# Performance work log

Hardware: AMD Instinct MI355X
Metric: run time of the kernel (lower is better)

The kernel has to match this reference:

```python
import jax, jax.numpy as jnp
import numpy as np

N_IMG = 1024
N_VIEWS = 90


def _bilinear(img, yi, xi):
    """Bilinear sample img at float coords (yi=row, xi=col); 0 outside (skimage warp cval=0)."""
    n = img.shape[0]
    y0 = jnp.floor(yi)
    x0 = jnp.floor(xi)
    wy = yi - y0
    wx = xi - x0
    y0i = y0.astype(jnp.int32)
    x0i = x0.astype(jnp.int32)

    def get(yy, xx):
        valid = (yy >= 0) & (yy < n) & (xx >= 0) & (xx < n)
        v = img[jnp.clip(yy, 0, n - 1), jnp.clip(xx, 0, n - 1)]
        return jnp.where(valid, v, jnp.zeros((), img.dtype))

    v00 = get(y0i, x0i)
    v01 = get(y0i, x0i + 1)
    v10 = get(y0i + 1, x0i)
    v11 = get(y0i + 1, x0i + 1)
    return (v00 * (1 - wy) * (1 - wx) + v01 * (1 - wy) * wx
            + v10 * wy * (1 - wx) + v11 * wy * wx)


def radon_jax(image, theta_deg):
    """skimage.transform.radon(image, theta, circle=True) equivalent.
    Rotate image by each angle (bilinear, about center = N//2, inverse map as in
    skimage warp) and sum over rows. Returns sinogram [N, n_angles]."""
    n = image.shape[0]
    center = n // 2
    ang = jnp.deg2rad(theta_deg.astype(image.dtype))
    cos_a = jnp.cos(ang)  # [A]
    sin_a = jnp.sin(ang)
    coords = jnp.arange(n, dtype=image.dtype)
    X, Y = jnp.meshgrid(coords, coords)  # X = col (x), Y = row (y), [N, N]

    def rotate_and_sum(ca, sa):
        # inverse map: src = R @ dst (homogeneous, (x, y) order) as in skimage radon
        x_in = ca * X + sa * Y - center * (ca + sa - 1)
        y_in = -sa * X + ca * Y - center * (ca - sa - 1)
        rotated = _bilinear(image, y_in, x_in)  # [N, N]
        return rotated.sum(axis=0)  # sum over rows -> projection [N]

    sino = jax.vmap(rotate_and_sum)(cos_a, sin_a)  # [A, N]
    return sino.T  # [N, A] to match skimage radon layout


def setup_inputs() -> dict:
    key = jax.random.key(0)
    k1, _ = jax.random.split(key)
    x = jax.random.normal(k1, (N_IMG, N_IMG), dtype=jnp.float32)
    theta = jnp.arange(N_VIEWS, dtype=jnp.float32) * 2.0  # 0..178 deg, 2-deg spacing
    return {"x": x, "theta": theta}


def reference(x, theta):
    return radon_jax(x, theta)
```

## Files before the change

### kernel.cpp

```cpp
#include <hip/hip_runtime.h>

#define N_IMG   1024
#define N_VIEWS 90
#define CENTER  512
#define TILE    64
#define NYB     (N_IMG / TILE)
#define NTHREADS 512
#define NWAVES   8
#define YPT      (TILE / NWAVES)
#define TILE_WORDS 9216

typedef float v2f __attribute__((ext_vector_type(2)));

__device__ __forceinline__ void map_coords(float ca, float sa, float cx, float cy,
                                           float Xf, float Yf,
                                           float& x_in, float& y_in) {
    const float fx0 = fmaf(ca, Xf, cx);
    const float fy0 = fmaf(-sa, Xf, cy);
    x_in = fmaf(sa, Yf, fx0);
    y_in = fmaf(ca, Yf, fy0);
}

__device__ __forceinline__ void gload_lds4(const float* g, float* l) {
    __builtin_amdgcn_global_load_lds((const __attribute__((address_space(1))) void*)g,
                                     (__attribute__((address_space(3))) void*)l, 4, 0, 0);
}
__device__ __forceinline__ void gload_lds16(const float* g, float* l) {
    __builtin_amdgcn_global_load_lds((const __attribute__((address_space(1))) void*)g,
                                     (__attribute__((address_space(3))) void*)l, 16, 0, 0);
}

template<int STRIDE>
__device__ __forceinline__ float sample_tile(const float* __restrict__ tile,
                                             float sa, float ca,
                                             float x_in, float y_in, float basef) {
    const float Sf = (float)STRIDE;
    v2f x2 = {x_in, x_in + sa};
    v2f y2 = {y_in, y_in + ca};
    const v2f dx2 = {2.0f * sa, 2.0f * sa};
    const v2f dy2 = {2.0f * ca, 2.0f * ca};
    const v2f S2  = {Sf, Sf};
    const v2f b2  = {basef, basef};
    v2f acc2 = {0.0f, 0.0f};
    #pragma unroll
    for (int p = 0; p < YPT / 2; ++p) {
        v2f x0f = {floorf(x2.x), floorf(x2.y)};
        v2f y0f = {floorf(y2.x), floorf(y2.y)};
        const v2f wx = x2 - x0f;
        const v2f wy = y2 - y0f;
        const v2f lif = y0f * S2 + x0f + b2;
        const int li0 = (int)lif.x;
        const int li1 = (int)lif.y;
        const v2f t00 = {tile[li0],              tile[li1]};
        const v2f t01 = {tile[li0 + 1],          tile[li1 + 1]};
        const v2f t10 = {tile[li0 + STRIDE],     tile[li1 + STRIDE]};
        const v2f t11 = {tile[li0 + STRIDE + 1], tile[li1 + STRIDE + 1]};
        const v2f top = (t01 - t00) * wx + t00;
        const v2f bot = (t11 - t10) * wx + t10;
        acc2 += (bot - top) * wy + top;
        x2 += dx2; y2 += dy2;
    }
    return acc2.x + acc2.y;
}

__global__ __launch_bounds__(NTHREADS) void radon_tile(const float* __restrict__ img,
                                                       const float* __restrict__ theta,
                                                       float* __restrict__ partial,
                                                       float* __restrict__ out,
                                                       int mode) {
    __shared__ float tile[TILE_WORDS];
    __shared__ float fpar[4];
    __shared__ int   ipar[8];

    const int a  = blockIdx.z;
    const int X0 = blockIdx.x * TILE;
    const int Y0 = blockIdx.y * TILE;
    const int tid  = threadIdx.x;
    const int lane = tid & 63;
    const int wv   = tid >> 6;

    if (wv == 0) {
        const float ang = theta[a] * 0.017453292519943295f;
        float sa, ca;
        __sincosf(ang, &sa, &ca);
        const float cx = (float)CENTER * (1.0f - ca - sa);
        const float cy = (float)CENTER * (1.0f - ca + sa);

        float x00, y00, x01, y01, x10, y10, x11, y11;
        map_coords(ca, sa, cx, cy, (float)X0,        (float)Y0,        x00, y00);
        map_coords(ca, sa, cx, cy, (float)(X0 + 63), (float)Y0,        x01, y01);
        map_coords(ca, sa, cx, cy, (float)X0,        (float)(Y0 + 63), x10, y10);
        map_coords(ca, sa, cx, cy, (float)(X0 + 63), (float)(Y0 + 63), x11, y11);
        const float xmin = fminf(fminf(x00, x01), fminf(x10, x11));
        const float xmax = fmaxf(fmaxf(x00, x01), fmaxf(x10, x11));
        const float ymin = fminf(fminf(y00, y01), fminf(y10, y11));
        const float ymax = fmaxf(fmaxf(y00, y01), fmaxf(y10, y11));

        const int ix0_raw = (int)floorf(xmin);
        const int ix1_raw = (int)floorf(xmax) + 1;
        const int iy0_raw = (int)floorf(ymin);
        const int iy1_raw = (int)floorf(ymax) + 1;

        const bool empty = (ix1_raw < 0) || (ix0_raw > N_IMG - 1) ||
                           (iy1_raw < 0) || (iy0_raw > N_IMG - 1);
        const bool interior = (ix0_raw >= 0) && (ix1_raw <= N_IMG - 1) &&
                              (iy0_raw >= 0) && (iy1_raw <= N_IMG - 1);

        int path = (fabsf(ca) > 0.7072f) ? 0 : ((ca > 0.0f) ? 1 : 2);
        int iy0w, win, dB = 0, ry0 = 0, nrows = 0;
        if (interior) {
            iy0w = iy0_raw;
            if (path == 0) {
                win = min(ix0_raw & ~3, N_IMG - 96);
            } else {
                win = min(ix0_raw, N_IMG - 64);
                dB  = max(win, ix1_raw - 63) - win;
            }
            nrows = iy1_raw - iy0_raw + 1;
        } else {
            iy0w = iy0_raw;
            win  = ix0_raw & ~3;
            ry0  = max(0, iy0_raw);
            nrows = min(N_IMG - 1, iy1_raw) - ry0 + 1;
        }
        if (tid == 0) {
            fpar[0] = sa; fpar[1] = ca; fpar[2] = cx; fpar[3] = cy;
            ipar[0] = iy0w; ipar[1] = nrows; ipar[2] = win; ipar[3] = dB;
            ipar[4] = path;
            ipar[5] = empty ? 1 : (interior ? 2 : 0);
            ipar[6] = ry0;
        }
    }
    __syncthreads();

    float* __restrict__ pslot = partial + ((size_t)(a * NYB + blockIdx.y) << 10) + X0;
    const int flags = ipar[5];

    if (flags & 1) {
        if (mode == 0 && tid < 64) pslot[tid] = 0.0f;
        return;
    }

    const float sa = fpar[0], ca = fpar[1], cx = fpar[2], cy = fpar[3];
    const int iy0 = ipar[0], nrows = ipar[1], win = ipar[2], dB = ipar[3];
    const int path = ipar[4];
    const int S = (path == 0) ? 96 : ((path == 1) ? 95 : 97);

    if (flags & 2) {
        if (path == 0) {
            const int D = nrows * 96;
            for (int o = wv * 256; o < D; o += NWAVES * 256) {
                const int d = o + 4 * lane;
                const int r = (unsigned)d / 96u;
                const int c = d - r * 96;
                const int gr = min(iy0 + r, N_IMG - 1);
                gload_lds16(img + (size_t)gr * N_IMG + win + c, tile + o);
            }
        } else {
            const float* g = img + (size_t)(iy0 + wv) * N_IMG + win + lane;
            float* l = tile + wv * S;
            for (int r = wv; r < nrows; r += NWAVES) {
                gload_lds4(g, l);
                if (dB > 0) gload_lds4(g + dB, l + dB);
                g += NWAVES * N_IMG;
                l += NWAVES * S;
            }
        }
    } else {
        for (int o4 = tid; o4 < TILE_WORDS / 4; o4 += NTHREADS)
            *(float4*)(tile + 4 * o4) = make_float4(0.f, 0.f, 0.f, 0.f);
        __syncthreads();
        const int ry0 = ipar[6];
        const int cx0 = max(0, win);
        const int cxe = min(N_IMG - 1, win + 94);
        const int wIn = cxe - cx0 + 1;
        const int n4  = wIn >> 2;
        const int items = nrows * 24;
        for (int idx = tid; idx < items; idx += NTHREADS) {
            const int r  = (unsigned)idx / 24u;
            const int c4 = idx - r * 24;
            const int gy = ry0 + r;
            float* dst = tile + (gy - iy0) * S + (cx0 - win) + 4 * c4;
            const float* src = img + (size_t)gy * N_IMG + cx0 + 4 * c4;
            if (c4 < n4) {
                *(float4*)dst = *(const float4*)src;
            } else if (c4 == n4) {
                for (int j = 0; j < (wIn & 3); ++j) dst[j] = src[j];
            }
        }
    }
    __syncthreads();

    const float Xf  = (float)(X0 + lane);
    const float fx0 = fmaf(ca, Xf, cx);
    const float fy0 = fmaf(-sa, Xf, cy);
    const float Ybf = (float)(Y0 + wv * YPT);
    const float x_in = fmaf(sa, Ybf, fx0);
    const float y_in = fmaf(ca, Ybf, fy0);
    const float basef = -(float)(iy0 * S + win);

    float acc;
    if (path == 0)      acc = sample_tile<96>(tile, sa, ca, x_in, y_in, basef);
    else if (path == 1) acc = sample_tile<95>(tile, sa, ca, x_in, y_in, basef);
    else                acc = sample_tile<97>(tile, sa, ca, x_in, y_in, basef);

    __syncthreads();
    tile[wv * 64 + lane] = acc;
    __syncthreads();
    if (wv == 0) {
        float s = 0.0f;
        #pragma unroll
        for (int w = 0; w < NWAVES; ++w) s += tile[w * 64 + lane];
        if (mode == 0) pslot[lane] = s;
        else           atomicAdd(&out[(X0 + lane) * N_VIEWS + a], s);
    }
}

__global__ __launch_bounds__(256) void reduce_partials(const float* __restrict__ partial,
                                                       float* __restrict__ out) {
    const int g = blockIdx.x * 256 + threadIdx.x;
    const int a = g >> 10;
    const int X = g & 1023;
    float s = 0.0f;
    #pragma unroll
    for (int yb = 0; yb < NYB; ++yb)
        s += partial[((size_t)(a * NYB + yb) << 10) + X];
    out[X * N_VIEWS + a] = s;
}

extern "C" void kernel_launch(void* const* d_in, const int* in_sizes, int n_in,
                              void* d_out, int out_size, void* d_ws, size_t ws_size,
                              hipStream_t stream) {
    const float* img   = (const float*)d_in[0];
    const float* theta = (const float*)d_in[1];
    float* out     = (float*)d_out;
    float* partial = (float*)d_ws;

    const size_t needed = (size_t)N_VIEWS * NYB * N_IMG * sizeof(float);
    const int mode = (ws_size >= needed) ? 0 : 1;
    if (mode == 1)
        (void)hipMemsetAsync(d_out, 0, (size_t)out_size * sizeof(float), stream);

    dim3 grid(N_IMG / TILE, N_IMG / TILE, N_VIEWS);
    radon_tile<<<grid, NTHREADS, 0, stream>>>(img, theta, partial, out, mode);

    if (mode == 0)
        reduce_partials<<<(N_VIEWS * N_IMG) / 256, 256, 0, stream>>>(partial, out);
}
```

Measured before the change: 140.0 us.

## Use transposed image copy for steep-angle tiles to avoid LDS bank conflicts

Adds a transpose kernel that writes a transposed copy of the image into workspace. For interior tiles whose angle would use the odd-stride paths and whose per-lane offsets would cause bank conflicts, the tile is now loaded from the transposed image with 16-byte global-to-LDS loads and a stride-96 layout. A transposed sampler swaps the x/y roles. This targets LDS bank conflicts and narrow 4-byte loads on near-vertical angles, at the cost of an extra transpose launch and more workspace.

```diff
diff --git a/kernel.cpp b/kernel.cpp
--- a/kernel.cpp
+++ b/kernel.cpp
@@ -28,6 +28,22 @@
 __device__ __forceinline__ void gload_lds16(const float* g, float* l) {
     __builtin_amdgcn_global_load_lds((const __attribute__((address_space(1))) void*)g,
                                      (__attribute__((address_space(3))) void*)l, 16, 0, 0);
+}
+
+__global__ __launch_bounds__(256) void transpose_img(const float* __restrict__ in,
+                                                     float* __restrict__ outT) {
+    __shared__ float t[32][33];
+    const int bx = blockIdx.x * 32;
+    const int by = blockIdx.y * 32;
+    const int lx = threadIdx.x & 31;
+    const int ly = threadIdx.x >> 5;
+    #pragma unroll
+    for (int i = 0; i < 32; i += 8)
+        t[ly + i][lx] = in[(size_t)(by + ly + i) * N_IMG + bx + lx];
+    __syncthreads();
+    #pragma unroll
+    for (int i = 0; i < 32; i += 8)
+        outT[(size_t)(bx + ly + i) * N_IMG + by + lx] = t[lx][ly + i];
 }
 
 template<int STRIDE>
@@ -63,11 +79,45 @@
     return acc2.x + acc2.y;
 }
 
+template<int STRIDE>
+__device__ __forceinline__ float sample_tileT(const float* __restrict__ tile,
+                                              float sa, float ca,
+                                              float x_in, float y_in, float basef) {
+    const float Sf = (float)STRIDE;
+    v2f x2 = {x_in, x_in + sa};
+    v2f y2 = {y_in, y_in + ca};
+    const v2f dx2 = {2.0f * sa, 2.0f * sa};
+    const v2f dy2 = {2.0f * ca, 2.0f * ca};
+    const v2f S2  = {Sf, Sf};
+    const v2f b2  = {basef, basef};
+    v2f acc2 = {0.0f, 0.0f};
+    #pragma unroll
+    for (int p = 0; p < YPT / 2; ++p) {
+        v2f x0f = {floorf(x2.x), floorf(x2.y)};
+        v2f y0f = {floorf(y2.x), floorf(y2.y)};
+        const v2f wx = x2 - x0f;
+        const v2f wy = y2 - y0f;
+        const v2f lif = x0f * S2 + y0f + b2;
+        const int li0 = (int)lif.x;
+        const int li1 = (int)lif.y;
+        const v2f t00 = {tile[li0],              tile[li1]};
+        const v2f t10 = {tile[li0 + 1],          tile[li1 + 1]};
+        const v2f t01 = {tile[li0 + STRIDE],     tile[li1 + STRIDE]};
+        const v2f t11 = {tile[li0 + STRIDE + 1], tile[li1 + STRIDE + 1]};
+        const v2f lft = (t10 - t00) * wy + t00;
+        const v2f rgt = (t11 - t01) * wy + t01;
+        acc2 += (rgt - lft) * wx + lft;
+        x2 += dx2; y2 += dy2;
+    }
+    return acc2.x + acc2.y;
+}
+
 __global__ __launch_bounds__(NTHREADS) void radon_tile(const float* __restrict__ img,
+                                                       const float* __restrict__ imgT,
                                                        const float* __restrict__ theta,
                                                        float* __restrict__ partial,
                                                        float* __restrict__ out,
-                                                       int mode) {
+                                                       int mode, int useT) {
     __shared__ float tile[TILE_WORDS];
     __shared__ float fpar[4];
     __shared__ int   ipar[8];
@@ -107,9 +157,9 @@
                               (iy0_raw >= 0) && (iy1_raw <= N_IMG - 1);
 
         int path = (fabsf(ca) > 0.7072f) ? 0 : ((ca > 0.0f) ? 1 : 2);
-        int iy0w, win, dB = 0, ry0 = 0, nrows = 0;
+        int row0, win, dB = 0, ry0 = 0, nrows = 0;
         if (interior) {
-            iy0w = iy0_raw;
+            row0 = iy0_raw;
             if (path == 0) {
                 win = min(ix0_raw & ~3, N_IMG - 96);
             } else {
@@ -117,15 +167,26 @@
                 dB  = max(win, ix1_raw - 63) - win;
             }
             nrows = iy1_raw - iy0_raw + 1;
+            if (useT && path != 0) {
+                const float tt = (96.0f * ca - sa) * 0.03125f;
+                const float fr = fabsf(tt - rintf(tt)) * 32.0f;
+                if (fr >= 1.0f) {
+                    path  = 3;
+                    row0  = ix0_raw;
+                    nrows = ix1_raw - ix0_raw + 1;
+                    win   = min(iy0_raw & ~3, N_IMG - 96);
+                    dB    = 0;
+                }
+            }
         } else {
-            iy0w = iy0_raw;
+            row0 = iy0_raw;
             win  = ix0_raw & ~3;
             ry0  = max(0, iy0_raw);
             nrows = min(N_IMG - 1, iy1_raw) - ry0 + 1;
         }
         if (tid == 0) {
             fpar[0] = sa; fpar[1] = ca; fpar[2] = cx; fpar[3] = cy;
-            ipar[0] = iy0w; ipar[1] = nrows; ipar[2] = win; ipar[3] = dB;
+            ipar[0] = row0; ipar[1] = nrows; ipar[2] = win; ipar[3] = dB;
             ipar[4] = path;
             ipar[5] = empty ? 1 : (interior ? 2 : 0);
             ipar[6] = ry0;
@@ -142,22 +203,23 @@
     }
 
     const float sa = fpar[0], ca = fpar[1], cx = fpar[2], cy = fpar[3];
-    const int iy0 = ipar[0], nrows = ipar[1], win = ipar[2], dB = ipar[3];
+    const int row0 = ipar[0], nrows = ipar[1], win = ipar[2], dB = ipar[3];
     const int path = ipar[4];
-    const int S = (path == 0) ? 96 : ((path == 1) ? 95 : 97);
+    const int S = (path == 1) ? 95 : ((path == 2) ? 97 : 96);
 
     if (flags & 2) {
-        if (path == 0) {
+        if (path == 0 || path == 3) {
+            const float* src = (path == 0) ? img : imgT;
             const int D = nrows * 96;
             for (int o = wv * 256; o < D; o += NWAVES * 256) {
                 const int d = o + 4 * lane;
                 const int r = (unsigned)d / 96u;
                 const int c = d - r * 96;
-                const int gr = min(iy0 + r, N_IMG - 1);
-                gload_lds16(img + (size_t)gr * N_IMG + win + c, tile + o);
+                const int gr = min(row0 + r, N_IMG - 1);
+                gload_lds16(src + (size_t)gr * N_IMG + win + c, tile + o);
             }
         } else {
-            const float* g = img + (size_t)(iy0 + wv) * N_IMG + win + lane;
+            const float* g = img + (size_t)(row0 + wv) * N_IMG + win + lane;
             float* l = tile + wv * S;
             for (int r = wv; r < nrows; r += NWAVES) {
                 gload_lds4(g, l);
@@ -180,7 +242,7 @@
             const int r  = (unsigned)idx / 24u;
             const int c4 = idx - r * 24;
             const int gy = ry0 + r;
-            float* dst = tile + (gy - iy0) * S + (cx0 - win) + 4 * c4;
+            float* dst = tile + (gy - row0) * S + (cx0 - win) + 4 * c4;
             const float* src = img + (size_t)gy * N_IMG + cx0 + 4 * c4;
             if (c4 < n4) {
                 *(float4*)dst = *(const float4*)src;
@@ -197,12 +259,13 @@
     const float Ybf = (float)(Y0 + wv * YPT);
     const float x_in = fmaf(sa, Ybf, fx0);
     const float y_in = fmaf(ca, Ybf, fy0);
-    const float basef = -(float)(iy0 * S + win);
+    const float basef = -(float)(row0 * S + win);
 
     float acc;
     if (path == 0)      acc = sample_tile<96>(tile, sa, ca, x_in, y_in, basef);
     else if (path == 1) acc = sample_tile<95>(tile, sa, ca, x_in, y_in, basef);
-    else                acc = sample_tile<97>(tile, sa, ca, x_in, y_in, basef);
+    else if (path == 2) acc = sample_tile<97>(tile, sa, ca, x_in, y_in, basef);
+    else                acc = sample_tileT<96>(tile, sa, ca, x_in, y_in, basef);
 
     __syncthreads();
     tile[wv * 64 + lane] = acc;
@@ -233,16 +296,25 @@
                               hipStream_t stream) {
     const float* img   = (const float*)d_in[0];
     const float* theta = (const float*)d_in[1];
-    float* out     = (float*)d_out;
-    float* partial = (float*)d_ws;
-
-    const size_t needed = (size_t)N_VIEWS * NYB * N_IMG * sizeof(float);
-    const int mode = (ws_size >= needed) ? 0 : 1;
+    float* out = (float*)d_out;
+
+    const size_t pbytes = (size_t)N_VIEWS * NYB * N_IMG * sizeof(float);
+    const size_t tbytes = (size_t)4 << 20;
+    const int useT = (ws_size >= tbytes + pbytes) ? 1 : 0;
+    float* imgT    = (float*)d_ws;
+    float* partial = useT ? (float*)((char*)d_ws + tbytes) : (float*)d_ws;
+    const int mode = (ws_size >= pbytes) ? 0 : 1;
     if (mode == 1)
         (void)hipMemsetAsync(d_out, 0, (size_t)out_size * sizeof(float), stream);
 
+    if (useT) {
+        dim3 tgrid(N_IMG / 32, N_IMG / 32);
+        transpose_img<<<tgrid, 256, 0, stream>>>(img, imgT);
+    }
+
     dim3 grid(N_IMG / TILE, N_IMG / TILE, N_VIEWS);
-    radon_tile<<<grid, NTHREADS, 0, stream>>>(img, theta, partial, out, mode);
+    radon_tile<<<grid, NTHREADS, 0, stream>>>(img, imgT, theta, partial, out,
+                                              mode, useT);
 
     if (mode == 0)
         reduce_partials<<<(N_VIEWS * N_IMG) / 256, 256, 0, stream>>>(partial, out);
```

Result: slower. 144.0 us (+2.8%).
